# Optimization experiments

Hardware: AMD Instinct MI355X
Metric: run time of the kernel (lower is better)

## Reference

```python
import jax, jax.numpy as jnp
import numpy as np

EMB = 256          # embedding_size
P = 2              # scoring_norm
EPS = 1e-6
APPLY_TANH = True
DIST_PER_DIM = True
N_REL = 1024
BATCH = 131072


def setup_inputs() -> dict:
    key = jax.random.key(0)
    k1, k2, k3, k4 = jax.random.split(key, 4)
    head_emb = jax.random.normal(k1, (BATCH, 2 * EMB), dtype=jnp.float32)
    tail_emb = jax.random.normal(k2, (BATCH, 2 * EMB), dtype=jnp.float32)
    relation_id = jax.random.randint(k3, (BATCH,), 0, N_REL, dtype=jnp.int32)
    # relation row = [center_h | center_t | width_h | width_t | size_h | size_t]
    relation_embedding = jax.random.uniform(k4, (N_REL, 4 * EMB + 2), dtype=jnp.float32)
    return {"head_emb": head_emb, "relation_id": relation_id,
            "tail_emb": tail_emb, "relation_embedding": relation_embedding}


def _boxe_score(bumped_ht, center_ht, width_ht, box_size):
    # bumped_ht/center_ht/width_ht: (B, 2, EMB); box_size: (B, 2)
    width = jnp.abs(width_ht)
    # geometric-mean normalization of box widths (softened by EPS)
    gmean = jnp.exp(jnp.mean(jnp.log(jnp.clip(width, EPS, None)), axis=-1, keepdims=True))
    width = width / jnp.clip(gmean, EPS, None)
    width = width * (1.0 + jax.nn.elu(box_size[..., None].astype(width.dtype)))
    if APPLY_TANH:
        width = jnp.tanh(width)
        center_ht = jnp.tanh(center_ht)
        bumped_ht = jnp.tanh(bumped_ht)
    width_p1 = width + 1.0
    center_dist = jnp.abs(bumped_ht - center_ht)
    # kappa = 0.5 * w * (w+1 - 1/(w+1))
    kappa = 0.5 * width * (width_p1 - 1.0 / width_p1)
    in_box = center_dist <= width / 2.0
    if not DIST_PER_DIM:
        in_box = jnp.all(in_box, axis=-1, keepdims=True)
    dist = jnp.where(in_box, center_dist / width_p1, center_dist * width_p1 - kappa)
    # p-norm over embedding dim -> (B, 2); negative sum of head+tail scores
    norm = jnp.power(jnp.sum(jnp.power(jnp.abs(dist), P), axis=-1), 1.0 / P)
    return -jnp.sum(norm, axis=-1)


def reference(head_emb, relation_id, tail_emb, relation_embedding):
    rel = relation_embedding[relation_id]                       # (B, 4*EMB+2)
    B = head_emb.shape[0]
    center_ht = rel[:, : 2 * EMB].reshape(B, 2, EMB)
    width_ht = rel[:, 2 * EMB : 4 * EMB].reshape(B, 2, EMB)
    box_size = rel[:, 4 * EMB :].reshape(B, 2)
    head_pos, head_bump = head_emb[:, :EMB], head_emb[:, EMB:]
    tail_pos, tail_bump = tail_emb[:, :EMB], tail_emb[:, EMB:]
    # bumped heads scored vs head box, bumped tails vs tail box
    bumped_ht = jnp.stack([head_pos + tail_bump, tail_pos + head_bump], axis=1)  # (B,2,EMB)
    return _boxe_score(bumped_ht, center_ht, width_ht, box_size)
```

## Files before the change

kernel.cpp:

```cpp
#include <hip/hip_runtime.h>
#include <hip/hip_fp16.h>

constexpr int EMB = 256;
constexpr int RELDIMS = 512;
constexpr float FEPS = 1e-6f;
constexpr int ROWS = 4;
constexpr int WPB  = 4;

typedef float f4 __attribute__((ext_vector_type(4)));

__device__ __forceinline__ float ftanh(float x) {
    x = fminf(15.f, fmaxf(-15.f, x));
    float t = __expf(2.f * x);
    return (t - 1.f) * __builtin_amdgcn_rcpf(t + 1.f);
}

__global__ __launch_bounds__(256) void boxe_pre(
    const float* __restrict__ rel, int n_rel, unsigned int* __restrict__ pre)
{
    const int r    = (blockIdx.x * blockDim.x + threadIdx.x) >> 6;
    const int lane = threadIdx.x & 63;
    if (r >= n_rel) return;
    const float* __restrict__ rrow = rel + (long)r * (4 * EMB + 2);
    const int d0 = lane * 4;

    float c0[4], c1[4], w0[4], w1[4];
    *(float4*)c0 = *(const float4*)(rrow + d0);
    *(float4*)c1 = *(const float4*)(rrow + EMB + d0);
    *(float4*)w0 = *(const float4*)(rrow + 2 * EMB + d0);
    *(float4*)w1 = *(const float4*)(rrow + 3 * EMB + d0);
    const float bs0 = rrow[4 * EMB + 0];
    const float bs1 = rrow[4 * EMB + 1];

    float wa0[4], wa1[4], ls0 = 0.f, ls1 = 0.f;
#pragma unroll
    for (int j = 0; j < 4; ++j) {
        wa0[j] = fabsf(w0[j]); wa1[j] = fabsf(w1[j]);
        ls0 += __logf(fmaxf(wa0[j], FEPS));
        ls1 += __logf(fmaxf(wa1[j], FEPS));
    }
#pragma unroll
    for (int off = 32; off >= 1; off >>= 1) {
        ls0 += __shfl_xor(ls0, off, 64);
        ls1 += __shfl_xor(ls1, off, 64);
    }
    const float g0 = __expf(ls0 * (1.f / (float)EMB));
    const float g1 = __expf(ls1 * (1.f / (float)EMB));
    const float e0 = (bs0 > 0.f) ? bs0 : (__expf(bs0) - 1.f);
    const float e1 = (bs1 > 0.f) ? bs1 : (__expf(bs1) - 1.f);
    const float s0 = (1.f + e0) / fmaxf(g0, FEPS);
    const float s1 = (1.f + e1) / fmaxf(g1, FEPS);

    unsigned int* __restrict__ prow = pre + (long)r * RELDIMS;
    unsigned int pk[4];
#pragma unroll
    for (int j = 0; j < 4; ++j) {
        __half2 h2 = __floats2half2_rn(ftanh(c0[j]), ftanh(wa0[j] * s0) + 1.f);
        pk[j] = *(unsigned int*)&h2;
    }
    *(uint4*)(prow + d0) = make_uint4(pk[0], pk[1], pk[2], pk[3]);
#pragma unroll
    for (int j = 0; j < 4; ++j) {
        __half2 h2 = __floats2half2_rn(ftanh(c1[j]), ftanh(wa1[j] * s1) + 1.f);
        pk[j] = *(unsigned int*)&h2;
    }
    *(uint4*)(prow + EMB + d0) = make_uint4(pk[0], pk[1], pk[2], pk[3]);
}

__global__ __launch_bounds__(256, 4) void boxe_main(
    const float* __restrict__ head, const int* __restrict__ rid,
    const float* __restrict__ tail, const unsigned int* __restrict__ pre,
    float* __restrict__ out)
{
    const int wave = blockIdx.x * WPB + (threadIdx.x >> 6);
    const int lane = threadIdx.x & 63;
    const int b0   = wave * ROWS;

    const int fidx = lane * 8;
    const int tidx = (lane ^ 32) * 8;

    int ridv[ROWS];
    {
        int4 ra = *(const int4*)(rid + b0);
        ridv[0] = ra.x; ridv[1] = ra.y; ridv[2] = ra.z; ridv[3] = ra.w;
    }

    f4    hbuf[3][2], tbuf[3][2];
    uint4 pbuf[3][2];

#define LOADROW(slot, i_)                                                     \
    {                                                                         \
        const float* hrow = head + (size_t)(b0 + (i_)) * RELDIMS;             \
        const float* trow = tail + (size_t)(b0 + (i_)) * RELDIMS;             \
        const unsigned int* prow = pre + (size_t)ridv[(i_)] * RELDIMS;        \
        hbuf[slot][0] = *(const f4*)(hrow + fidx);                            \
        hbuf[slot][1] = *(const f4*)(hrow + fidx + 4);                        \
        tbuf[slot][0] = *(const f4*)(trow + tidx);                            \
        tbuf[slot][1] = *(const f4*)(trow + tidx + 4);                        \
        pbuf[slot][0] = *(const uint4*)(prow + fidx);                         \
        pbuf[slot][1] = *(const uint4*)(prow + fidx + 4);                     \
    }

    LOADROW(0, 0)
    LOADROW(1, 1)

#pragma unroll
    for (int i = 0; i < ROWS; ++i) {
        const int cur = i % 3;
        if (i + 2 < ROWS) {
            const int nxt = (i + 2) % 3;
            LOADROW(nxt, i + 2)
        }

        float h[8], t[8];
        unsigned int pw[8];
        *(f4*)(h)     = hbuf[cur][0]; *(f4*)(h + 4) = hbuf[cur][1];
        *(f4*)(t)     = tbuf[cur][0]; *(f4*)(t + 4) = tbuf[cur][1];
        *(uint4*)(pw) = pbuf[cur][0]; *(uint4*)(pw + 4) = pbuf[cur][1];

        float acc = 0.f;
#pragma unroll
        for (int j = 0; j < 8; ++j) {
            float2 cw = __half22float2(*(__half2*)&pw[j]);
            float ct = cw.x, wp1 = cw.y;
            float bt  = ftanh(h[j] + t[j]);
            float cd  = fabsf(bt - ct);
            float wv  = wp1 - 1.f;
            float inv = __builtin_amdgcn_rcpf(wp1);
            float kap = 0.5f * wv * (wp1 - inv);
            float d   = (cd <= 0.5f * wv) ? (cd * inv) : fmaf(cd, wp1, -kap);
            acc = fmaf(d, d, acc);
        }
#pragma unroll
        for (int off = 16; off >= 1; off >>= 1)
            acc += __shfl_xor(acc, off, 64);
        float other = __shfl_xor(acc, 32, 64);
        if (lane == 0) out[b0 + i] = -(sqrtf(acc) + sqrtf(other));
    }
#undef LOADROW
}

__device__ __forceinline__ float dist2_term(float wabs, float scale, float c, float bm) {
    float w   = ftanh(wabs * scale);
    float ctv = ftanh(c);
    float bt  = ftanh(bm);
    float cd  = fabsf(bt - ctv);
    float wp1 = w + 1.f;
    float inv = __builtin_amdgcn_rcpf(wp1);
    float kappa = 0.5f * w * (wp1 - inv);
    float dist = (cd <= 0.5f * w) ? (cd * inv) : fmaf(cd, wp1, -kappa);
    return dist * dist;
}

__global__ __launch_bounds__(256) void boxe_fused(
    const float* __restrict__ head, const int* __restrict__ rid,
    const float* __restrict__ tail, const float* __restrict__ rel,
    float* __restrict__ out, int batch)
{
    const int b    = (int)(((size_t)blockIdx.x * blockDim.x + threadIdx.x) >> 6);
    const int lane = threadIdx.x & 63;
    if (b >= batch) return;
    const long r = rid[b];
    const float* __restrict__ rrow = rel  + r * (long)(4 * EMB + 2);
    const float* __restrict__ hrow = head + (long)b * RELDIMS;
    const float* __restrict__ trow = tail + (long)b * RELDIMS;
    const int d0 = lane * 4;
    float hp[4], hb[4], tp[4], tb[4], c0[4], c1[4], w0[4], w1[4];
    *(float4*)hp = *(const float4*)(hrow + d0);
    *(float4*)hb = *(const float4*)(hrow + EMB + d0);
    *(float4*)tp = *(const float4*)(trow + d0);
    *(float4*)tb = *(const float4*)(trow + EMB + d0);
    *(float4*)c0 = *(const float4*)(rrow + d0);
    *(float4*)c1 = *(const float4*)(rrow + EMB + d0);
    *(float4*)w0 = *(const float4*)(rrow + 2 * EMB + d0);
    *(float4*)w1 = *(const float4*)(rrow + 3 * EMB + d0);
    const float bs0 = rrow[4 * EMB + 0];
    const float bs1 = rrow[4 * EMB + 1];
    float wa0[4], wa1[4], ls0 = 0.f, ls1 = 0.f;
#pragma unroll
    for (int j = 0; j < 4; ++j) {
        wa0[j] = fabsf(w0[j]); wa1[j] = fabsf(w1[j]);
        ls0 += __logf(fmaxf(wa0[j], FEPS)); ls1 += __logf(fmaxf(wa1[j], FEPS));
    }
#pragma unroll
    for (int off = 32; off >= 1; off >>= 1) {
        ls0 += __shfl_xor(ls0, off, 64); ls1 += __shfl_xor(ls1, off, 64);
    }
    const float g0 = __expf(ls0 * (1.f / 256.f)), g1 = __expf(ls1 * (1.f / 256.f));
    const float e0 = (bs0 > 0.f) ? bs0 : (__expf(bs0) - 1.f);
    const float e1 = (bs1 > 0.f) ? bs1 : (__expf(bs1) - 1.f);
    const float s0 = (1.f + e0) / fmaxf(g0, FEPS);
    const float s1 = (1.f + e1) / fmaxf(g1, FEPS);
    float acc0 = 0.f, acc1 = 0.f;
#pragma unroll
    for (int j = 0; j < 4; ++j) {
        acc0 += dist2_term(wa0[j], s0, c0[j], hp[j] + tb[j]);
        acc1 += dist2_term(wa1[j], s1, c1[j], tp[j] + hb[j]);
    }
#pragma unroll
    for (int off = 32; off >= 1; off >>= 1) {
        acc0 += __shfl_xor(acc0, off, 64); acc1 += __shfl_xor(acc1, off, 64);
    }
    if (lane == 0) out[b] = -(sqrtf(acc0) + sqrtf(acc1));
}

extern "C" void kernel_launch(void* const* d_in, const int* in_sizes, int n_in,
                              void* d_out, int out_size, void* d_ws, size_t ws_size,
                              hipStream_t stream) {
    const float* head = (const float*)d_in[0];
    const int*   rid  = (const int*)d_in[1];
    const float* tail = (const float*)d_in[2];
    const float* rel  = (const float*)d_in[3];
    float* out = (float*)d_out;

    const int batch = out_size;
    const int n_rel = in_sizes[3] / (4 * EMB + 2);
    const size_t need = (size_t)n_rel * RELDIMS * sizeof(unsigned int);

    if (ws_size >= need && batch % (WPB * ROWS) == 0) {
        unsigned int* pre = (unsigned int*)d_ws;
        boxe_pre<<<(n_rel + 3) / 4, 256, 0, stream>>>(rel, n_rel, pre);
        const int blocks = batch / (WPB * ROWS);
        boxe_main<<<blocks, 256, 0, stream>>>(head, rid, tail, pre, out);
    } else {
        const int blocks = (batch + 3) / 4;
        boxe_fused<<<blocks, 256, 0, stream>>>(head, rid, tail, rel, out, batch);
    }
}
```

Baseline: 106.4 us.

## Process two rows per wave with all loads issued upfront instead of pipelined four

Replaces the four-rows-per-wave kernel and its three-slot software pipeline with a two-rows-per-wave kernel that issues every load for both rows at the start and computes four independent accumulators. Each lane now covers one head-box and one tail-box slice of 4 dims rather than 8 contiguous dims with a swizzled tail index, and the two results are written with a single float2 store. Launch bounds rise to 6 waves per SIMD and the grid doubles, trading per-wave pipelining for more resident waves to hide memory latency in this bandwidth-bound kernel.

```diff
diff --git a/kernel.cpp b/kernel.cpp
--- a/kernel.cpp
+++ b/kernel.cpp
@@ -4,8 +4,8 @@
 constexpr int EMB = 256;
 constexpr int RELDIMS = 512;
 constexpr float FEPS = 1e-6f;
-constexpr int ROWS = 4;
-constexpr int WPB  = 4;
+constexpr int RPW = 2;
+constexpr int WPB = 4;
 
 typedef float f4 __attribute__((ext_vector_type(4)));
 
@@ -67,77 +67,106 @@
     *(uint4*)(prow + EMB + d0) = make_uint4(pk[0], pk[1], pk[2], pk[3]);
 }
 
-__global__ __launch_bounds__(256, 4) void boxe_main(
+__global__ __launch_bounds__(256, 6) void boxe_main(
     const float* __restrict__ head, const int* __restrict__ rid,
     const float* __restrict__ tail, const unsigned int* __restrict__ pre,
     float* __restrict__ out)
 {
     const int wave = blockIdx.x * WPB + (threadIdx.x >> 6);
     const int lane = threadIdx.x & 63;
-    const int b0   = wave * ROWS;
-
-    const int fidx = lane * 8;
-    const int tidx = (lane ^ 32) * 8;
-
-    int ridv[ROWS];
-    {
-        int4 ra = *(const int4*)(rid + b0);
-        ridv[0] = ra.x; ridv[1] = ra.y; ridv[2] = ra.z; ridv[3] = ra.w;
-    }
-
-    f4    hbuf[3][2], tbuf[3][2];
-    uint4 pbuf[3][2];
-
-#define LOADROW(slot, i_)                                                     \
-    {                                                                         \
-        const float* hrow = head + (size_t)(b0 + (i_)) * RELDIMS;             \
-        const float* trow = tail + (size_t)(b0 + (i_)) * RELDIMS;             \
-        const unsigned int* prow = pre + (size_t)ridv[(i_)] * RELDIMS;        \
-        hbuf[slot][0] = *(const f4*)(hrow + fidx);                            \
-        hbuf[slot][1] = *(const f4*)(hrow + fidx + 4);                        \
-        tbuf[slot][0] = *(const f4*)(trow + tidx);                            \
-        tbuf[slot][1] = *(const f4*)(trow + tidx + 4);                        \
-        pbuf[slot][0] = *(const uint4*)(prow + fidx);                         \
-        pbuf[slot][1] = *(const uint4*)(prow + fidx + 4);                     \
-    }
-
-    LOADROW(0, 0)
-    LOADROW(1, 1)
-
-#pragma unroll
-    for (int i = 0; i < ROWS; ++i) {
-        const int cur = i % 3;
-        if (i + 2 < ROWS) {
-            const int nxt = (i + 2) % 3;
-            LOADROW(nxt, i + 2)
-        }
-
-        float h[8], t[8];
-        unsigned int pw[8];
-        *(f4*)(h)     = hbuf[cur][0]; *(f4*)(h + 4) = hbuf[cur][1];
-        *(f4*)(t)     = tbuf[cur][0]; *(f4*)(t + 4) = tbuf[cur][1];
-        *(uint4*)(pw) = pbuf[cur][0]; *(uint4*)(pw + 4) = pbuf[cur][1];
-
-        float acc = 0.f;
-#pragma unroll
-        for (int j = 0; j < 8; ++j) {
-            float2 cw = __half22float2(*(__half2*)&pw[j]);
-            float ct = cw.x, wp1 = cw.y;
-            float bt  = ftanh(h[j] + t[j]);
-            float cd  = fabsf(bt - ct);
-            float wv  = wp1 - 1.f;
-            float inv = __builtin_amdgcn_rcpf(wp1);
-            float kap = 0.5f * wv * (wp1 - inv);
-            float d   = (cd <= 0.5f * wv) ? (cd * inv) : fmaf(cd, wp1, -kap);
-            acc = fmaf(d, d, acc);
-        }
-#pragma unroll
-        for (int off = 16; off >= 1; off >>= 1)
-            acc += __shfl_xor(acc, off, 64);
-        float other = __shfl_xor(acc, 32, 64);
-        if (lane == 0) out[b0 + i] = -(sqrtf(acc) + sqrtf(other));
-    }
-#undef LOADROW
+    const int b0   = wave * RPW;
+    const int d0   = lane * 4;
+
+    const int2 rr = *(const int2*)(rid + b0);
+
+    const float* __restrict__ h0 = head + (size_t)b0 * RELDIMS;
+    const float* __restrict__ t0 = tail + (size_t)b0 * RELDIMS;
+    const float* __restrict__ h1 = h0 + RELDIMS;
+    const float* __restrict__ t1 = t0 + RELDIMS;
+    const unsigned int* __restrict__ p0 = pre + (size_t)rr.x * RELDIMS;
+    const unsigned int* __restrict__ p1 = pre + (size_t)rr.y * RELDIMS;
+
+    f4 hp0 = *(const f4*)(h0 + d0);
+    f4 hb0 = *(const f4*)(h0 + EMB + d0);
+    f4 tp0 = *(const f4*)(t0 + d0);
+    f4 tb0 = *(const f4*)(t0 + EMB + d0);
+    uint4 pa0 = *(const uint4*)(p0 + d0);
+    uint4 pb0 = *(const uint4*)(p0 + EMB + d0);
+    f4 hp1 = *(const f4*)(h1 + d0);
+    f4 hb1 = *(const f4*)(h1 + EMB + d0);
+    f4 tp1 = *(const f4*)(t1 + d0);
+    f4 tb1 = *(const f4*)(t1 + EMB + d0);
+    uint4 pa1 = *(const uint4*)(p1 + d0);
+    uint4 pb1 = *(const uint4*)(p1 + EMB + d0);
+
+    float a00 = 0.f, a01 = 0.f, a10 = 0.f, a11 = 0.f;
+
+    const unsigned int pwa0[4] = {pa0.x, pa0.y, pa0.z, pa0.w};
+    const unsigned int pwb0[4] = {pb0.x, pb0.y, pb0.z, pb0.w};
+    const unsigned int pwa1[4] = {pa1.x, pa1.y, pa1.z, pa1.w};
+    const unsigned int pwb1[4] = {pb1.x, pb1.y, pb1.z, pb1.w};
+
+#pragma unroll
+    for (int j = 0; j < 4; ++j) {
+        {
+            float2 cw = __half22float2(*(const __half2*)&pwa0[j]);
+            float ct = cw.x, wp1 = cw.y;
+            float bt  = ftanh(hp0[j] + tb0[j]);
+            float cd  = fabsf(bt - ct);
+            float wv  = wp1 - 1.f;
+            float inv = __builtin_amdgcn_rcpf(wp1);
+            float kap = 0.5f * wv * (wp1 - inv);
+            float d   = (cd <= 0.5f * wv) ? (cd * inv) : fmaf(cd, wp1, -kap);
+            a00 = fmaf(d, d, a00);
+        }
+        {
+            float2 cw = __half22float2(*(const __half2*)&pwb0[j]);
+            float ct = cw.x, wp1 = cw.y;
+            float bt  = ftanh(tp0[j] + hb0[j]);
+            float cd  = fabsf(bt - ct);
+            float wv  = wp1 - 1.f;
+            float inv = __builtin_amdgcn_rcpf(wp1);
+            float kap = 0.5f * wv * (wp1 - inv);
+            float d   = (cd <= 0.5f * wv) ? (cd * inv) : fmaf(cd, wp1, -kap);
+            a01 = fmaf(d, d, a01);
+        }
+        {
+            float2 cw = __half22float2(*(const __half2*)&pwa1[j]);
+            float ct = cw.x, wp1 = cw.y;
+            float bt  = ftanh(hp1[j] + tb1[j]);
+            float cd  = fabsf(bt - ct);
+            float wv  = wp1 - 1.f;
+            float inv = __builtin_amdgcn_rcpf(wp1);
+            float kap = 0.5f * wv * (wp1 - inv);
+            float d   = (cd <= 0.5f * wv) ? (cd * inv) : fmaf(cd, wp1, -kap);
+            a10 = fmaf(d, d, a10);
+        }
+        {
+            float2 cw = __half22float2(*(const __half2*)&pwb1[j]);
+            float ct = cw.x, wp1 = cw.y;
+            float bt  = ftanh(tp1[j] + hb1[j]);
+            float cd  = fabsf(bt - ct);
+            float wv  = wp1 - 1.f;
+            float inv = __builtin_amdgcn_rcpf(wp1);
+            float kap = 0.5f * wv * (wp1 - inv);
+            float d   = (cd <= 0.5f * wv) ? (cd * inv) : fmaf(cd, wp1, -kap);
+            a11 = fmaf(d, d, a11);
+        }
+    }
+
+#pragma unroll
+    for (int off = 32; off >= 1; off >>= 1) {
+        a00 += __shfl_xor(a00, off, 64);
+        a01 += __shfl_xor(a01, off, 64);
+        a10 += __shfl_xor(a10, off, 64);
+        a11 += __shfl_xor(a11, off, 64);
+    }
+    if (lane == 0) {
+        float2 o;
+        o.x = -(sqrtf(a00) + sqrtf(a01));
+        o.y = -(sqrtf(a10) + sqrtf(a11));
+        *(float2*)(out + b0) = o;
+    }
 }
 
 __device__ __forceinline__ float dist2_term(float wabs, float scale, float c, float bm) {
@@ -217,10 +246,10 @@
     const int n_rel = in_sizes[3] / (4 * EMB + 2);
     const size_t need = (size_t)n_rel * RELDIMS * sizeof(unsigned int);
 
-    if (ws_size >= need && batch % (WPB * ROWS) == 0) {
+    if (ws_size >= need && batch % (WPB * RPW) == 0) {
         unsigned int* pre = (unsigned int*)d_ws;
         boxe_pre<<<(n_rel + 3) / 4, 256, 0, stream>>>(rel, n_rel, pre);
-        const int blocks = batch / (WPB * ROWS);
+        const int blocks = batch / (WPB * RPW);
         boxe_main<<<blocks, 256, 0, stream>>>(head, rid, tail, pre, out);
     } else {
         const int blocks = (batch + 3) / 4;
```

Result: no change. 106.7 us (+0.3%).
